# Optimization experiments

Hardware: AMD Instinct MI355X
Metric: run time of the kernel (lower is better)

Reference implementation:

```python
import jax, jax.numpy as jnp
import numpy as np

EMBED_DIM = 768
NUM_HEADS = 12
HEAD_DIM = EMBED_DIM // NUM_HEADS
SEQ_LEN = 196
NUM_CLASSES = 3
BATCH = 256


def setup_inputs() -> dict:
    key = jax.random.key(0)
    ks = jax.random.split(key, 7)
    s = 0.02
    return {
        "x": jax.random.normal(ks[0], (BATCH, SEQ_LEN * EMBED_DIM), dtype=jnp.float32),
        "qkv_w": jax.random.normal(ks[1], (EMBED_DIM, 3 * EMBED_DIM), dtype=jnp.float32) * s,
        "qkv_b": jax.random.normal(ks[2], (3 * EMBED_DIM,), dtype=jnp.float32) * s,
        "out_w": jax.random.normal(ks[3], (EMBED_DIM, EMBED_DIM), dtype=jnp.float32) * s,
        "out_b": jax.random.normal(ks[4], (EMBED_DIM,), dtype=jnp.float32) * s,
        "cls_w": jax.random.normal(ks[5], (SEQ_LEN * EMBED_DIM, NUM_CLASSES), dtype=jnp.float32) * s,
        "cls_b": jax.random.normal(ks[6], (NUM_CLASSES,), dtype=jnp.float32) * s,
    }


def reference(x, qkv_w, qkv_b, out_w, out_b, cls_w, cls_b):
    B = x.shape[0]
    # (B, S*E) -> (B, S, E)
    xt = x.reshape(B, SEQ_LEN, EMBED_DIM)
    # QKV projection: (B, S, 3E) -> (B, S, H, 3*hd)
    qkv = (xt @ qkv_w + qkv_b).reshape(B, SEQ_LEN, NUM_HEADS, 3 * HEAD_DIM)
    q, k, v = jnp.split(qkv, 3, axis=-1)  # each (B, S, H, hd)
    # NOTE: faithful to source — attention is over the HEADS axis (HxH per token),
    # because q @ k.transpose(-2,-1) acts on the last two dims of (B,S,H,hd).
    scale = 1.0 / (HEAD_DIM ** 0.5)
    scores = jnp.einsum("bsid,bsjd->bsij", q, k) * scale  # (B, S, H, H)
    attn = jax.nn.softmax(scores, axis=-1)
    out = jnp.einsum("bsij,bsjd->bsid", attn, v).reshape(B, SEQ_LEN, EMBED_DIM)
    out = out @ out_w + out_b                 # (B, S, E)
    out = out.reshape(B, SEQ_LEN * EMBED_DIM)  # flatten(1)
    return out @ cls_w + cls_b                # (B, num_classes)
```

## Files before the change

### kernel.cpp

```cpp
#include <hip/hip_runtime.h>

typedef _Float16 f16;
typedef _Float16 f16x8 __attribute__((ext_vector_type(8)));
typedef float f32x4 __attribute__((ext_vector_type(4)));

#define SEQ   196
#define EMB   768
#define NHEAD 12
#define HD    64
#define BATCH 256
#define TOK   (BATCH*SEQ)
#define QKVN  (3*EMB)
#define CLSK  (SEQ*EMB)

__global__ __launch_bounds__(256) void k_cvt8(const float* __restrict__ in,
                                              f16* __restrict__ out, int n8) {
  int i = blockIdx.x * 256 + threadIdx.x;
  if (i >= n8) return;
  const float4* p = (const float4*)in + (size_t)i * 2;
  float4 a = p[0], b = p[1];
  f16x8 o;
  o[0]=(f16)a.x; o[1]=(f16)a.y; o[2]=(f16)a.z; o[3]=(f16)a.w;
  o[4]=(f16)b.x; o[5]=(f16)b.y; o[6]=(f16)b.z; o[7]=(f16)b.w;
  *((f16x8*)out + i) = o;
}

__global__ __launch_bounds__(256) void k_transpose_cvt(const float* __restrict__ W,
                                                       f16* __restrict__ WT,
                                                       int K, int N) {
  __shared__ float tile[32][33];
  int n0 = blockIdx.x * 32, k0 = blockIdx.y * 32;
  int t = threadIdx.x, tx = t & 31, ty = t >> 5;
  #pragma unroll
  for (int i = 0; i < 4; ++i) {
    int r = ty + i * 8;
    tile[r][tx] = W[(size_t)(k0 + r) * N + n0 + tx];
  }
  __syncthreads();
  #pragma unroll
  for (int i = 0; i < 4; ++i) {
    int r = ty + i * 8;
    WT[(size_t)(n0 + r) * K + k0 + tx] = (f16)tile[tx][r];
  }
}

__global__ __launch_bounds__(256) void k_extract_cls(const float* __restrict__ cls_w,
                                                     f16* __restrict__ cls16,
                                                     float* __restrict__ zbias) {
  int idx = blockIdx.x * 256 + threadIdx.x;
  int r = idx / EMB, e = idx - r * EMB;
  int c = r / SEQ, s = r - c * SEQ;
  cls16[(size_t)r * EMB + e] = (f16)cls_w[((size_t)s * EMB + e) * 3 + c];
  if (blockIdx.x == 0)
    for (int i = threadIdx.x; i < EMB; i += 256) zbias[i] = 0.f;
}

__global__ __launch_bounds__(256) void k_const3a(const float* __restrict__ out_b,
                                                 const float* __restrict__ cls_w,
                                                 float* __restrict__ partial) {
  int s = blockIdx.x, t = threadIdx.x;
  float a0 = 0.f, a1 = 0.f, a2 = 0.f;
  for (int e = t; e < EMB; e += 256) {
    float ob = out_b[e];
    const float* p = cls_w + ((size_t)s * EMB + e) * 3;
    a0 += ob * p[0]; a1 += ob * p[1]; a2 += ob * p[2];
  }
  __shared__ float r0[256], r1[256], r2[256];
  r0[t] = a0; r1[t] = a1; r2[t] = a2;
  __syncthreads();
  for (int off = 128; off > 0; off >>= 1) {
    if (t < off) { r0[t] += r0[t + off]; r1[t] += r1[t + off]; r2[t] += r2[t + off]; }
    __syncthreads();
  }
  if (t == 0) { partial[s * 3 + 0] = r0[0]; partial[s * 3 + 1] = r1[0]; partial[s * 3 + 2] = r2[0]; }
}

__global__ __launch_bounds__(64) void k_const3b(const float* __restrict__ partial,
                                                const float* __restrict__ cls_b,
                                                float* __restrict__ const3) {
  int t = threadIdx.x;
  #pragma unroll
  for (int c = 0; c < 3; ++c) {
    float s = 0.f;
    for (int j = t; j < SEQ; j += 64) s += partial[j * 3 + c];
    #pragma unroll
    for (int off = 32; off > 0; off >>= 1) s += __shfl_down(s, off, 64);
    if (t == 0) const3[c] = s + cls_b[c];
  }
}

__global__ __launch_bounds__(256) void k_interleave(const f16* __restrict__ W2c,
                                                    float* __restrict__ W2i) {
  int idx = blockIdx.x * 256 + threadIdx.x;
  int r = idx / EMB, e = idx - r * EMB;
  int c = r / SEQ, s = r - c * SEQ;
  W2i[((size_t)s * EMB + e) * 3 + c] = (float)W2c[(size_t)r * EMB + e];
}

__global__ __launch_bounds__(256) void k_gemm_bias(
    const f16* __restrict__ A, const f16* __restrict__ Bm,
    const float* __restrict__ bias, f16* __restrict__ C,
    int M, int N, int K) {
  __shared__ f16 As[128 * 64];
  __shared__ f16 Bs[128 * 64];
  const int t = threadIdx.x;
  const int l = t & 63;
  const int w = t >> 6;
  const int wr = w >> 1, wc = w & 1;

  const int nwg = gridDim.x;
  const int orig = blockIdx.x;
  const int q = nwg >> 3, r8 = nwg & 7;
  const int xcd = orig & 7, seq = orig >> 3;
  const int base = xcd < r8 ? xcd * (q + 1) : r8 * (q + 1) + (xcd - r8) * q;
  const int wg = base + seq;
  const int NB = N >> 7;
  const int bm = wg / NB, bn = wg - bm * NB;

  const size_t rowA0 = (size_t)bm * 128, rowB0 = (size_t)bn * 128;

  f32x4 acc[4][4] = {};

  for (int k0 = 0; k0 < K; k0 += 64) {
    if (k0) __syncthreads();
    #pragma unroll
    for (int i = 0; i < 4; ++i) {
      int qq = i * 256 + t;
      int rr = qq >> 3, c = qq & 7;
      int cs = c ^ (rr & 7);
      const f16* ga = A  + (rowA0 + rr) * K + k0 + cs * 8;
      const f16* gb = Bm + (rowB0 + rr) * K + k0 + cs * 8;
      f16* la = As + (size_t)(i * 256 + w * 64) * 8;
      f16* lb = Bs + (size_t)(i * 256 + w * 64) * 8;
      __builtin_amdgcn_global_load_lds((const __attribute__((address_space(1))) void*)ga,
                                       (__attribute__((address_space(3))) void*)la, 16, 0, 0);
      __builtin_amdgcn_global_load_lds((const __attribute__((address_space(1))) void*)gb,
                                       (__attribute__((address_space(3))) void*)lb, 16, 0, 0);
    }
    __syncthreads();
    #pragma unroll
    for (int ks = 0; ks < 2; ++ks) {
      f16x8 av[4], bv[4];
      const int k8 = ks * 4 + (l >> 4);
      #pragma unroll
      for (int m = 0; m < 4; ++m) {
        int rr = wr * 64 + m * 16 + (l & 15);
        av[m] = *(const f16x8*)((const char*)As + rr * 128 + ((k8 ^ (rr & 7)) << 4));
      }
      #pragma unroll
      for (int n = 0; n < 4; ++n) {
        int rr = wc * 64 + n * 16 + (l & 15);
        bv[n] = *(const f16x8*)((const char*)Bs + rr * 128 + ((k8 ^ (rr & 7)) << 4));
      }
      #pragma unroll
      for (int m = 0; m < 4; ++m)
        #pragma unroll
        for (int n = 0; n < 4; ++n)
          acc[m][n] = __builtin_amdgcn_mfma_f32_16x16x32_f16(av[m], bv[n], acc[m][n], 0, 0, 0);
    }
  }
  #pragma unroll
  for (int n = 0; n < 4; ++n) {
    int gcol = bn * 128 + wc * 64 + n * 16 + (l & 15);
    float bs = bias[gcol];
    #pragma unroll
    for (int m = 0; m < 4; ++m) {
      int grow0 = bm * 128 + wr * 64 + m * 16 + (l >> 4) * 4;
      #pragma unroll
      for (int j = 0; j < 4; ++j)
        C[(size_t)(grow0 + j) * N + gcol] = (f16)(acc[m][n][j] + bs);
    }
  }
}

__global__ __launch_bounds__(64) void k_attn(const f16* __restrict__ qkv,
                                             f16* __restrict__ aout) {
  const int tok = blockIdx.x;
  const int l = threadIdx.x;
  __shared__ f16 row[QKVN];
  __shared__ float sc[144];
  __shared__ float aw[144];
  const uint2* src = (const uint2*)(qkv + (size_t)tok * QKVN);
  uint2* dst = (uint2*)row;
  #pragma unroll
  for (int i = 0; i < 9; ++i) dst[l + i * 64] = src[l + i * 64];
  __syncthreads();
  for (int p = l; p < 144; p += 64) {
    int i = p / 12, j = p - i * 12;
    const f16x8* q8 = (const f16x8*)(row + i * 192);
    const f16x8* k8 = (const f16x8*)(row + j * 192 + 64);
    float s = 0.f;
    #pragma unroll
    for (int d8 = 0; d8 < 8; ++d8) {
      f16x8 a = q8[d8], b = k8[d8];
      #pragma unroll
      for (int e = 0; e < 8; ++e) s += (float)a[e] * (float)b[e];
    }
    sc[p] = s * 0.125f;
  }
  __syncthreads();
  if (l < 12) {
    float m = -1e30f;
    #pragma unroll
    for (int j = 0; j < 12; ++j) m = fmaxf(m, sc[l * 12 + j]);
    float e[12], sum = 0.f;
    #pragma unroll
    for (int j = 0; j < 12; ++j) { e[j] = __expf(sc[l * 12 + j] - m); sum += e[j]; }
    float inv = 1.f / sum;
    #pragma unroll
    for (int j = 0; j < 12; ++j) aw[l * 12 + j] = e[j] * inv;
  }
  __syncthreads();
  float vv[12];
  #pragma unroll
  for (int j = 0; j < 12; ++j) vv[j] = (float)row[j * 192 + 128 + l];
  f16* op = aout + (size_t)tok * EMB;
  #pragma unroll
  for (int i = 0; i < 12; ++i) {
    float o = 0.f;
    #pragma unroll
    for (int j = 0; j < 12; ++j) o += aw[i * 12 + j] * vv[j];
    op[i * 64 + l] = (f16)o;
  }
}

__global__ __launch_bounds__(256) void k_cls2f(const f16* __restrict__ attno,
                                               const float* __restrict__ W2i,
                                               const float* __restrict__ const3,
                                               float* __restrict__ logits) {
  const int b = blockIdx.x, t = threadIdx.x;
  const f16* r = attno + (size_t)b * CLSK;
  float s0 = 0.f, s1 = 0.f, s2 = 0.f;
  for (int c8 = t; c8 < CLSK / 8; c8 += 256) {
    f16x8 v = *((const f16x8*)r + c8);
    float wv[24];
    const float4* wp = (const float4*)(W2i + (size_t)c8 * 24);
    #pragma unroll
    for (int i = 0; i < 6; ++i) *(float4*)&wv[i * 4] = wp[i];
    #pragma unroll
    for (int e = 0; e < 8; ++e) {
      float f = (float)v[e];
      s0 += f * wv[e * 3 + 0];
      s1 += f * wv[e * 3 + 1];
      s2 += f * wv[e * 3 + 2];
    }
  }
  __shared__ float r0[256], r1[256], r2[256];
  r0[t] = s0; r1[t] = s1; r2[t] = s2;
  __syncthreads();
  for (int off = 128; off > 0; off >>= 1) {
    if (t < off) { r0[t] += r0[t + off]; r1[t] += r1[t + off]; r2[t] += r2[t + off]; }
    __syncthreads();
  }
  if (t == 0) {
    logits[b * 3 + 0] = r0[0] + const3[0];
    logits[b * 3 + 1] = r1[0] + const3[1];
    logits[b * 3 + 2] = r2[0] + const3[2];
  }
}

extern "C" void kernel_launch(void* const* d_in, const int* in_sizes, int n_in,
                              void* d_out, int out_size, void* d_ws, size_t ws_size,
                              hipStream_t stream) {
  (void)in_sizes; (void)n_in; (void)out_size;
  const float* x      = (const float*)d_in[0];
  const float* qkv_w  = (const float*)d_in[1];
  const float* qkv_b  = (const float*)d_in[2];
  const float* out_w  = (const float*)d_in[3];
  const float* out_b  = (const float*)d_in[4];
  const float* cls_w  = (const float*)d_in[5];
  const float* cls_b  = (const float*)d_in[6];
  float* logits = (float*)d_out;

  const size_t SZ_X16 = (size_t)TOK * EMB * 2;
  const size_t SZ_QKV = (size_t)TOK * QKVN * 2;
  const size_t SZ_QT  = (size_t)QKVN * EMB * 2;
  const size_t SZ_OT  = (size_t)EMB * EMB * 2;
  if (ws_size < SZ_X16 + SZ_QKV + SZ_QT + SZ_OT) return;

  char* ws = (char*)d_ws;
  const size_t base2 = SZ_X16 + SZ_QKV;
  f16* x16      = (f16*)ws;
  f16* qkvb     = (f16*)(ws + SZ_X16);
  f16* qkvT     = (f16*)(ws + base2);
  f16* outw16   = (f16*)(ws + base2);
  f16* cls16    = (f16*)(ws + base2 + 1179648);
  f16* W2c      = (f16*)(ws + base2 + 2162688);
  float* W2i    = (float*)(ws + SZ_X16);
  float* partial= (float*)(ws + SZ_X16 + 2097152);
  float* zbias  = (float*)(ws + base2 + SZ_QT);
  float* const3 = (float*)(ws + base2 + SZ_QT + 3072);
  f16* attno = x16;

  k_cvt8<<<dim3(TOK * EMB / 8 / 256), dim3(256), 0, stream>>>(x, x16, TOK * EMB / 8);
  k_transpose_cvt<<<dim3(QKVN / 32, EMB / 32), dim3(256), 0, stream>>>(qkv_w, qkvT, EMB, QKVN);
  k_gemm_bias<<<dim3((TOK / 128) * (QKVN / 128)), dim3(256), 0, stream>>>(x16, qkvT, qkv_b, qkvb, TOK, QKVN, EMB);
  k_attn<<<dim3(TOK), dim3(64), 0, stream>>>(qkvb, attno);
  k_cvt8<<<dim3(EMB * EMB / 8 / 256), dim3(256), 0, stream>>>(out_w, outw16, EMB * EMB / 8);
  k_extract_cls<<<dim3(588 * EMB / 256), dim3(256), 0, stream>>>(cls_w, cls16, zbias);
  k_const3a<<<dim3(SEQ), dim3(256), 0, stream>>>(out_b, cls_w, partial);
  k_const3b<<<dim3(1), dim3(64), 0, stream>>>(partial, cls_b, const3);
  k_gemm_bias<<<dim3((640 / 128) * (EMB / 128)), dim3(256), 0, stream>>>(cls16, outw16, zbias, W2c, 640, EMB, EMB);
  k_interleave<<<dim3(588 * EMB / 256), dim3(256), 0, stream>>>(W2c, W2i);
  k_cls2f<<<dim3(BATCH), dim3(256), 0, stream>>>(attno, W2i, const3, logits);
}
```

Measured before the change: 393.0 us.

## Fuse fp32->fp16 conversion into QKV GEMM and fold classifier into attention

The separate x conversion pass is removed. The QKV GEMM now loads fp32 x directly, converts it in registers and writes it to LDS, prefetching the next A tile during MFMA. The attention kernel no longer writes the attention output. It dots each token's result with a padded folded classifier weight and emits per-token partial logits, which a small kernel reduces per batch. This cuts a large fp16 round trip through memory, at the cost of doubling the A-operand global traffic and using register-staged loads instead of direct-to-LDS loads.

```diff
diff --git a/kernel.cpp b/kernel.cpp
--- a/kernel.cpp
+++ b/kernel.cpp
@@ -12,6 +12,10 @@
 #define TOK   (BATCH*SEQ)
 #define QKVN  (3*EMB)
 #define CLSK  (SEQ*EMB)
+
+#define GLD16(gp, lp) __builtin_amdgcn_global_load_lds( \
+    (const __attribute__((address_space(1))) void*)(gp), \
+    (__attribute__((address_space(3))) void*)(lp), 16, 0, 0)
 
 __global__ __launch_bounds__(256) void k_cvt8(const float* __restrict__ in,
                                               f16* __restrict__ out, int n8) {
@@ -89,12 +93,12 @@
   }
 }
 
-__global__ __launch_bounds__(256) void k_interleave(const f16* __restrict__ W2c,
-                                                    float* __restrict__ W2i) {
+__global__ __launch_bounds__(256) void k_make_w2p(const f16* __restrict__ W2c,
+                                                  float* __restrict__ W2p) {
   int idx = blockIdx.x * 256 + threadIdx.x;
   int r = idx / EMB, e = idx - r * EMB;
   int c = r / SEQ, s = r - c * SEQ;
-  W2i[((size_t)s * EMB + e) * 3 + c] = (float)W2c[(size_t)r * EMB + e];
+  W2p[((size_t)s * EMB + e) * 4 + c] = (float)W2c[idx];
 }
 
 __global__ __launch_bounds__(256) void k_gemm_bias(
@@ -118,7 +122,6 @@
   const int bm = wg / NB, bn = wg - bm * NB;
 
   const size_t rowA0 = (size_t)bm * 128, rowB0 = (size_t)bn * 128;
-
   f32x4 acc[4][4] = {};
 
   for (int k0 = 0; k0 < K; k0 += 64) {
@@ -132,10 +135,8 @@
       const f16* gb = Bm + (rowB0 + rr) * K + k0 + cs * 8;
       f16* la = As + (size_t)(i * 256 + w * 64) * 8;
       f16* lb = Bs + (size_t)(i * 256 + w * 64) * 8;
-      __builtin_amdgcn_global_load_lds((const __attribute__((address_space(1))) void*)ga,
-                                       (__attribute__((address_space(3))) void*)la, 16, 0, 0);
-      __builtin_amdgcn_global_load_lds((const __attribute__((address_space(1))) void*)gb,
-                                       (__attribute__((address_space(3))) void*)lb, 16, 0, 0);
+      GLD16(ga, la);
+      GLD16(gb, lb);
     }
     __syncthreads();
     #pragma unroll
@@ -173,9 +174,99 @@
   }
 }
 
-__global__ __launch_bounds__(64) void k_attn(const f16* __restrict__ qkv,
-                                             f16* __restrict__ aout) {
-  const int tok = blockIdx.x;
+__global__ __launch_bounds__(256) void k_gemm_xa(
+    const float* __restrict__ A, const f16* __restrict__ Bm,
+    const float* __restrict__ bias, f16* __restrict__ C,
+    int M, int N, int K) {
+  __shared__ f16 As[128 * 64];
+  __shared__ f16 Bs[128 * 64];
+  const int t = threadIdx.x;
+  const int l = t & 63;
+  const int w = t >> 6;
+  const int wr = w >> 1, wc = w & 1;
+
+  const int nwg = gridDim.x;
+  const int orig = blockIdx.x;
+  const int q = nwg >> 3, r8 = nwg & 7;
+  const int xcd = orig & 7, seq = orig >> 3;
+  const int base = xcd < r8 ? xcd * (q + 1) : r8 * (q + 1) + (xcd - r8) * q;
+  const int wg = base + seq;
+  const int NB = N >> 7;
+  const int bm = wg / NB, bn = wg - bm * NB;
+
+  const size_t rowA0 = (size_t)bm * 128, rowB0 = (size_t)bn * 128;
+  f32x4 acc[4][4] = {};
+
+  float4 ua[4], va[4];
+  auto loadA = [&](int k0) {
+    #pragma unroll
+    for (int i = 0; i < 4; ++i) {
+      int qq = i * 256 + t;
+      int rr = qq >> 3, c = qq & 7;
+      int cs = c ^ (rr & 7);
+      const float4* g = (const float4*)(A + (rowA0 + rr) * (size_t)K + k0 + cs * 8);
+      ua[i] = g[0]; va[i] = g[1];
+    }
+  };
+
+  loadA(0);
+  for (int k0 = 0; k0 < K; k0 += 64) {
+    if (k0) __syncthreads();
+    #pragma unroll
+    for (int i = 0; i < 4; ++i) {
+      int qq = i * 256 + t;
+      f16x8 h;
+      h[0]=(f16)ua[i].x; h[1]=(f16)ua[i].y; h[2]=(f16)ua[i].z; h[3]=(f16)ua[i].w;
+      h[4]=(f16)va[i].x; h[5]=(f16)va[i].y; h[6]=(f16)va[i].z; h[7]=(f16)va[i].w;
+      *(f16x8*)(As + (size_t)qq * 8) = h;
+      int rr = qq >> 3, c = qq & 7;
+      int cs = c ^ (rr & 7);
+      const f16* gb = Bm + (rowB0 + rr) * (size_t)K + k0 + cs * 8;
+      f16* lb = Bs + (size_t)(i * 256 + w * 64) * 8;
+      GLD16(gb, lb);
+    }
+    __syncthreads();
+    if (k0 + 64 < K) loadA(k0 + 64);
+    #pragma unroll
+    for (int ks = 0; ks < 2; ++ks) {
+      f16x8 av[4], bv[4];
+      const int k8 = ks * 4 + (l >> 4);
+      #pragma unroll
+      for (int m = 0; m < 4; ++m) {
+        int rr = wr * 64 + m * 16 + (l & 15);
+        av[m] = *(const f16x8*)((const char*)As + rr * 128 + ((k8 ^ (rr & 7)) << 4));
+      }
+      #pragma unroll
+      for (int n = 0; n < 4; ++n) {
+        int rr = wc * 64 + n * 16 + (l & 15);
+        bv[n] = *(const f16x8*)((const char*)Bs + rr * 128 + ((k8 ^ (rr & 7)) << 4));
+      }
+      #pragma unroll
+      for (int m = 0; m < 4; ++m)
+        #pragma unroll
+        for (int n = 0; n < 4; ++n)
+          acc[m][n] = __builtin_amdgcn_mfma_f32_16x16x32_f16(av[m], bv[n], acc[m][n], 0, 0, 0);
+    }
+  }
+  #pragma unroll
+  for (int n = 0; n < 4; ++n) {
+    int gcol = bn * 128 + wc * 64 + n * 16 + (l & 15);
+    float bs = bias[gcol];
+    #pragma unroll
+    for (int m = 0; m < 4; ++m) {
+      int grow0 = bm * 128 + wr * 64 + m * 16 + (l >> 4) * 4;
+      #pragma unroll
+      for (int j = 0; j < 4; ++j)
+        C[(size_t)(grow0 + j) * N + gcol] = (f16)(acc[m][n][j] + bs);
+    }
+  }
+}
+
+__global__ __launch_bounds__(64) void k_attn_cls(const f16* __restrict__ qkv,
+                                                 const float* __restrict__ W2p,
+                                                 float* __restrict__ part4) {
+  const int s = blockIdx.x, b = blockIdx.y;
+  const int tok = b * SEQ + s;
   const int l = threadIdx.x;
   __shared__ f16 row[QKVN];
   __shared__ float sc[144];
@@ -189,14 +280,14 @@
     int i = p / 12, j = p - i * 12;
     const f16x8* q8 = (const f16x8*)(row + i * 192);
     const f16x8* k8 = (const f16x8*)(row + j * 192 + 64);
-    float s = 0.f;
+    float sv = 0.f;
     #pragma unroll
     for (int d8 = 0; d8 < 8; ++d8) {
-      f16x8 a = q8[d8], b = k8[d8];
-      #pragma unroll
-      for (int e = 0; e < 8; ++e) s += (float)a[e] * (float)b[e];
-    }
-    sc[p] = s * 0.125f;
+      f16x8 a = q8[d8], bb = k8[d8];
+      #pragma unroll
+      for (int e = 0; e < 8; ++e) sv += (float)a[e] * (float)bb[e];
+    }
+    sc[p] = sv * 0.125f;
   }
   __syncthreads();
   if (l < 12) {
@@ -214,48 +305,44 @@
   float vv[12];
   #pragma unroll
   for (int j = 0; j < 12; ++j) vv[j] = (float)row[j * 192 + 128 + l];
-  f16* op = aout + (size_t)tok * EMB;
+  const float4* wrow = (const float4*)W2p + (size_t)s * EMB;
+  float s0 = 0.f, s1 = 0.f, s2 = 0.f;
   #pragma unroll
   for (int i = 0; i < 12; ++i) {
     float o = 0.f;
     #pragma unroll
     for (int j = 0; j < 12; ++j) o += aw[i * 12 + j] * vv[j];
-    op[i * 64 + l] = (f16)o;
-  }
-}
-
-__global__ __launch_bounds__(256) void k_cls2f(const f16* __restrict__ attno,
-                                               const float* __restrict__ W2i,
-                                               const float* __restrict__ const3,
-                                               float* __restrict__ logits) {
-  const int b = blockIdx.x, t = threadIdx.x;
-  const f16* r = attno + (size_t)b * CLSK;
+    float4 wv = wrow[i * 64 + l];
+    s0 += o * wv.x; s1 += o * wv.y; s2 += o * wv.z;
+  }
+  #pragma unroll
+  for (int off = 32; off > 0; off >>= 1) {
+    s0 += __shfl_down(s0, off, 64);
+    s1 += __shfl_down(s1, off, 64);
+    s2 += __shfl_down(s2, off, 64);
+  }
+  if (l == 0) *(float4*)(part4 + (size_t)tok * 4) = make_float4(s0, s1, s2, 0.f);
+}
+
+__global__ __launch_bounds__(64) void k_cls_final(const float* __restrict__ part4,
+                                                  const float* __restrict__ const3,
+                                                  float* __restrict__ logits) {
+  const int b = blockIdx.x, l = threadIdx.x;
   float s0 = 0.f, s1 = 0.f, s2 = 0.f;
-  for (int c8 = t; c8 < CLSK / 8; c8 += 256) {
-    f16x8 v = *((const f16x8*)r + c8);
-    float wv[24];
-    const float4* wp = (const float4*)(W2i + (size_t)c8 * 24);
-    #pragma unroll
-    for (int i = 0; i < 6; ++i) *(float4*)&wv[i * 4] = wp[i];
-    #pragma unroll
-    for (int e = 0; e < 8; ++e) {
-      float f = (float)v[e];
-      s0 += f * wv[e * 3 + 0];
-      s1 += f * wv[e * 3 + 1];
-      s2 += f * wv[e * 3 + 2];
-    }
-  }
-  __shared__ float r0[256], r1[256], r2[256];
-  r0[t] = s0; r1[t] = s1; r2[t] = s2;
-  __syncthreads();
-  for (int off = 128; off > 0; off >>= 1) {
-    if (t < off) { r0[t] += r0[t + off]; r1[t] += r1[t + off]; r2[t] += r2[t + off]; }
-    __syncthreads();
-  }
-  if (t == 0) {
-    logits[b * 3 + 0] = r0[0] + const3[0];
-    logits[b * 3 + 1] = r1[0] + const3[1];
-    logits[b * 3 + 2] = r2[0] + const3[2];
+  for (int j = l; j < SEQ; j += 64) {
+    float4 p = *(const float4*)(part4 + ((size_t)b * SEQ + j) * 4);
+    s0 += p.x; s1 += p.y; s2 += p.z;
+  }
+  #pragma unroll
+  for (int off = 32; off > 0; off >>= 1) {
+    s0 += __shfl_down(s0, off, 64);
+    s1 += __shfl_down(s1, off, 64);
+    s2 += __shfl_down(s2, off, 64);
+  }
+  if (l == 0) {
+    logits[b * 3 + 0] = s0 + const3[0];
+    logits[b * 3 + 1] = s1 + const3[1];
+    logits[b * 3 + 2] = s2 + const3[2];
   }
 }
 
@@ -280,27 +367,25 @@
 
   char* ws = (char*)d_ws;
   const size_t base2 = SZ_X16 + SZ_QKV;
-  f16* x16      = (f16*)ws;
-  f16* qkvb     = (f16*)(ws + SZ_X16);
-  f16* qkvT     = (f16*)(ws + base2);
-  f16* outw16   = (f16*)(ws + base2);
-  f16* cls16    = (f16*)(ws + base2 + 1179648);
-  f16* W2c      = (f16*)(ws + base2 + 2162688);
-  float* W2i    = (float*)(ws + SZ_X16);
-  float* partial= (float*)(ws + SZ_X16 + 2097152);
-  float* zbias  = (float*)(ws + base2 + SZ_QT);
-  float* const3 = (float*)(ws + base2 + SZ_QT + 3072);
-  f16* attno = x16;
-
-  k_cvt8<<<dim3(TOK * EMB / 8 / 256), dim3(256), 0, stream>>>(x, x16, TOK * EMB / 8);
+  float* W2p     = (float*)(ws);
+  f16*   outw16  = (f16*)(ws + (4u << 20));
+  f16*   cls16   = (f16*)(ws + (8u << 20));
+  f16*   W2c     = (f16*)(ws + (12u << 20));
+  float* partial = (float*)(ws + (16u << 20));
+  float* part4   = (float*)(ws + (20u << 20));
+  float* zbias   = (float*)(ws + (24u << 20));
+  float* const3  = (float*)(ws + (25u << 20));
+  f16*   qkvb    = (f16*)(ws + SZ_X16);
+  f16*   qkvT    = (f16*)(ws + base2);
+
   k_transpose_cvt<<<dim3(QKVN / 32, EMB / 32), dim3(256), 0, stream>>>(qkv_w, qkvT, EMB, QKVN);
-  k_gemm_bias<<<dim3((TOK / 128) * (QKVN / 128)), dim3(256), 0, stream>>>(x16, qkvT, qkv_b, qkvb, TOK, QKVN, EMB);
-  k_attn<<<dim3(TOK), dim3(64), 0, stream>>>(qkvb, attno);
   k_cvt8<<<dim3(EMB * EMB / 8 / 256), dim3(256), 0, stream>>>(out_w, outw16, EMB * EMB / 8);
   k_extract_cls<<<dim3(588 * EMB / 256), dim3(256), 0, stream>>>(cls_w, cls16, zbias);
   k_const3a<<<dim3(SEQ), dim3(256), 0, stream>>>(out_b, cls_w, partial);
   k_const3b<<<dim3(1), dim3(64), 0, stream>>>(partial, cls_b, const3);
   k_gemm_bias<<<dim3((640 / 128) * (EMB / 128)), dim3(256), 0, stream>>>(cls16, outw16, zbias, W2c, 640, EMB, EMB);
-  k_interleave<<<dim3(588 * EMB / 256), dim3(256), 0, stream>>>(W2c, W2i);
-  k_cls2f<<<dim3(BATCH), dim3(256), 0, stream>>>(attno, W2i, const3, logits);
-}
+  k_make_w2p<<<dim3(588 * EMB / 256), dim3(256), 0, stream>>>(W2c, W2p);
+  k_gemm_xa<<<dim3((TOK / 128) * (QKVN / 128)), dim3(256), 0, stream>>>(x, qkvT, qkv_b, qkvb, TOK, QKVN, EMB);
+  k_attn_cls<<<dim3(SEQ, BATCH), dim3(64), 0, stream>>>(qkvb, W2p, part4);
+  k_cls_final<<<dim3(BATCH), dim3(64), 0, stream>>>(part4, const3, logits);
+}
```

Result: no change. 391.5 us (-0.4%).
